# Kernel tuning notes

Hardware: AMD Instinct MI355X
Metric: run time of the kernel (lower is better)

Reference implementation:

```python
import jax, jax.numpy as jnp
import numpy as np

N_HEAD = 16


def setup_inputs() -> dict:
    key = jax.random.key(0)
    ks = jax.random.split(key, 5)
    B, S, D = 4, 2048, 1024
    scale = 1.0 / np.sqrt(D)
    return {
        "x": jax.random.normal(ks[0], (B, S, D), dtype=jnp.float32),
        "Wq": jax.random.normal(ks[1], (D, D), dtype=jnp.float32) * scale,
        "bq": jnp.zeros((D,), dtype=jnp.float32),
        "Wk": jax.random.normal(ks[2], (D, D), dtype=jnp.float32) * scale,
        "bk": jnp.zeros((D,), dtype=jnp.float32),
        "Wv": jax.random.normal(ks[3], (D, D), dtype=jnp.float32) * scale,
        "bv": jnp.zeros((D,), dtype=jnp.float32),
        "Wo": jax.random.normal(ks[4], (D, D), dtype=jnp.float32) * scale,
        "bo": jnp.zeros((D,), dtype=jnp.float32),
    }


def reference(x, Wq, bq, Wk, bk, Wv, bv, Wo, bo):
    B, S, D = x.shape
    H = N_HEAD
    Dh = D // H
    # projections (torch Linear == x @ W^T + b; here W stored as (in, out))
    q = (x @ Wq + bq).reshape(B, S, H, Dh).transpose(0, 2, 1, 3)  # (B,H,S,Dh)
    k = (x @ Wk + bk).reshape(B, S, H, Dh).transpose(0, 2, 1, 3)
    v = (x @ Wv + bv).reshape(B, S, H, Dh).transpose(0, 2, 1, 3)
    scores = jnp.einsum("bhsd,bhtd->bhst", q, k) / jnp.sqrt(jnp.float32(Dh))
    causal = jnp.tril(jnp.ones((S, S), dtype=bool))  # (S,S)
    scores = jnp.where(causal[None, None], scores, -jnp.inf)
    weights = jax.nn.softmax(scores, axis=-1)  # (B,H,S,S)
    attn = jnp.einsum("bhst,bhtd->bhsd", weights, v)
    attn = attn.transpose(0, 2, 1, 3).reshape(B, S, D)
    out = attn @ Wo + bo
    return out
```

## Files before the change

kernel.cpp:

```cpp
#include <hip/hip_runtime.h>
#include <hip/hip_bf16.h>


typedef __bf16 bf16x8 __attribute__((ext_vector_type(8)));
typedef float f32x4 __attribute__((ext_vector_type(4)));
typedef unsigned short u16;

__device__ __forceinline__ u16 f2b(float f) {
    __hip_bfloat16 h = __float2bfloat16(f);
    return __builtin_bit_cast(unsigned short, h);
}

__device__ __forceinline__ f32x4 mfma16(bf16x8 a, bf16x8 b, f32x4 c) {
    return __builtin_amdgcn_mfma_f32_16x16x32_bf16(a, b, c, 0, 0, 0);
}

typedef const __attribute__((address_space(1))) unsigned int* gas1_t;
typedef __attribute__((address_space(3))) unsigned int* las3_t;
__device__ __forceinline__ void gld16(const void* g, void* l) {
    __builtin_amdgcn_global_load_lds((gas1_t)g, (las3_t)l, 16, 0, 0);
}

__global__ __launch_bounds__(256) void convert_x(const float* __restrict__ x,
                                                 u16* __restrict__ xb, int n4) {
    int i = blockIdx.x * 256 + threadIdx.x;
    if (i < n4) {
        float4 v = ((const float4*)x)[i];
        ushort4 u;
        u.x = f2b(v.x); u.y = f2b(v.y); u.z = f2b(v.z); u.w = f2b(v.w);
        ((ushort4*)xb)[i] = u;
    }
}

__global__ __launch_bounds__(256) void transpose_w(const float* __restrict__ Wq,
                                                   const float* __restrict__ Wk,
                                                   const float* __restrict__ Wv,
                                                   const float* __restrict__ Wo,
                                                   u16* __restrict__ wqkvt,
                                                   u16* __restrict__ wot) {
    const int z = blockIdx.z;
    const float* src = (z == 0) ? Wq : (z == 1) ? Wk : (z == 2) ? Wv : Wo;
    u16* dst = (z == 3) ? wot : (wqkvt + (size_t)z * 1024 * 1024);
    __shared__ float tile[32][33];
    const int tx = threadIdx.x, ty = threadIdx.y;
    const int nbase = blockIdx.x * 32, kbase = blockIdx.y * 32;
    for (int j = 0; j < 4; ++j)
        tile[ty + j * 8][tx] = src[(size_t)(kbase + ty + j * 8) * 1024 + nbase + tx];
    __syncthreads();
    for (int j = 0; j < 4; ++j)
        dst[(size_t)(nbase + ty + j * 8) * 1024 + kbase + tx] = f2b(tile[tx][ty + j * 8]);
}

__global__ __launch_bounds__(256) void pack_bqkv(const float* __restrict__ bq,
                                                 const float* __restrict__ bk,
                                                 const float* __restrict__ bv,
                                                 float* __restrict__ bqkv) {
    int i = blockIdx.x * 256 + threadIdx.x;
    bqkv[i] = (i < 1024) ? bq[i] : (i < 2048) ? bk[i - 1024] : bv[i - 2048];
}

template <int MODE>
__global__ __launch_bounds__(256, 2) void gemm_bt(const u16* __restrict__ A,
                                                  const u16* __restrict__ Bt,
                                                  const float* __restrict__ bias,
                                                  void* __restrict__ Cout,
                                                  void* __restrict__ Cout2,
                                                  int M, int N, int K, int ldc) {
    const int tid = threadIdx.x;
    const int l = tid & 63;
    const int w = tid >> 6;
    const int tileM = blockIdx.x * 128;
    const int tileN = blockIdx.y * 128;

    __shared__ u16 As[2][128 * 32];
    __shared__ u16 Bs[2][128 * 32];

    const int srow = l >> 2;
    const int schunk = l & 3;
    const int mrow = l & 15;
    const int g8 = (l >> 4) * 8;
    const int waveM = (w & 1) * 64;
    const int waveN = (w >> 1) * 64;

    const u16* a0 = A + (size_t)(tileM + w * 32 + srow) * K + schunk * 8;
    const u16* a1 = A + (size_t)(tileM + w * 32 + 16 + srow) * K + schunk * 8;
    const u16* b0 = Bt + (size_t)(tileN + w * 32 + srow) * K + schunk * 8;
    const u16* b1 = Bt + (size_t)(tileN + w * 32 + 16 + srow) * K + schunk * 8;

    f32x4 acc[4][4] = {};

    gld16(a0, &As[0][(w * 2) * 512]);
    gld16(a1, &As[0][(w * 2 + 1) * 512]);
    gld16(b0, &Bs[0][(w * 2) * 512]);
    gld16(b1, &Bs[0][(w * 2 + 1) * 512]);
    __syncthreads();

    for (int k0 = 0; k0 < K; k0 += 32) {
        const int cur = (k0 >> 5) & 1;
        if (k0 + 32 < K) {
            const int nb = cur ^ 1;
            gld16(a0 + k0 + 32, &As[nb][(w * 2) * 512]);
            gld16(a1 + k0 + 32, &As[nb][(w * 2 + 1) * 512]);
            gld16(b0 + k0 + 32, &Bs[nb][(w * 2) * 512]);
            gld16(b1 + k0 + 32, &Bs[nb][(w * 2 + 1) * 512]);
        }

        bf16x8 af[4], bf[4];
        for (int im = 0; im < 4; ++im)
            af[im] = *(const bf16x8*)&As[cur][(waveM + im * 16 + mrow) * 32 + g8];
        for (int in = 0; in < 4; ++in)
            bf[in] = *(const bf16x8*)&Bs[cur][(waveN + in * 16 + mrow) * 32 + g8];
        for (int im = 0; im < 4; ++im)
            for (int in = 0; in < 4; ++in)
                acc[im][in] = mfma16(af[im], bf[in], acc[im][in]);
        __syncthreads();
    }

    const int rbase = (l >> 4) * 4;
    for (int im = 0; im < 4; ++im) {
        for (int in = 0; in < 4; ++in) {
            const int gm0 = tileM + waveM + im * 16 + rbase;
            const int gn = tileN + waveN + in * 16 + (l & 15);
            const float bv_ = bias[gn];
            if (MODE == 1) {
                float* out = (float*)Cout;
                for (int r = 0; r < 4; ++r)
                    out[(size_t)(gm0 + r) * ldc + gn] = acc[im][in][r] + bv_;
            } else if (tileN < 2048) {
                const float qs = (tileN < 1024) ? 0.125f * 1.4426950408889634f : 1.0f;
                u16* out = (u16*)Cout;
                for (int r = 0; r < 4; ++r)
                    out[(size_t)(gm0 + r) * 2048 + gn] = f2b((acc[im][in][r] + bv_) * qs);
            } else {
                u16* out = (u16*)Cout2;
                const int b = gm0 >> 11, s0 = gm0 & 2047;
                const int gn2 = gn - 2048;
                const int h = gn2 >> 6, dh = gn2 & 63;
                ushort4 u;
                u.x = f2b(acc[im][in][0] + bv_);
                u.y = f2b(acc[im][in][1] + bv_);
                u.z = f2b(acc[im][in][2] + bv_);
                u.w = f2b(acc[im][in][3] + bv_);
                *(ushort4*)&out[((size_t)((b * 16 + h) * 64 + dh)) * 2048 + s0] = u;
            }
        }
    }
}

__global__ __launch_bounds__(256, 2) void attn_kernel(const u16* __restrict__ qk,
                                                      const u16* __restrict__ vt,
                                                      u16* __restrict__ attn) {
    const int bh = blockIdx.x;
    const int qt = 15 - (int)blockIdx.y;
    const int b = bh >> 4, h = bh & 15;
    const int q0 = qt * 128;
    const int tid = threadIdx.x, l = tid & 63, w = tid >> 6;
    const int q = l & 15;
    const int g = l >> 4;
    const int g8 = g * 8;

    __shared__ u16 Ks[2][64 * 64];
    __shared__ u16 Vs[2][64 * 64];
    __shared__ u16 Ps[128 * 72];

    const int sr8 = l >> 3;
    const int gc = (l & 7) ^ sr8;
    const u16* kgl = qk + (size_t)(b * 2048 + w * 16 + sr8) * 2048 + 1024 + h * 64 + gc * 8;
    const u16* vgl = vt + (size_t)(bh * 64 + w * 16 + sr8) * 2048 + gc * 8;

    for (int i = 0; i < 4; ++i) {
        const int idx = i * 256 + tid;
        const int row = idx >> 3, ch = idx & 7;
        *(uint4*)&Ps[row * 72 + ch * 8] =
            *(const uint4*)&qk[(size_t)(b * 2048 + q0 + row) * 2048 + h * 64 + ch * 8];
    }
    for (int j = 0; j < 2; ++j) {
        gld16(kgl + (size_t)(j * 8) * 2048, &Ks[0][(w * 16 + j * 8) * 64]);
        gld16(vgl + (size_t)(j * 8) * 2048, &Vs[0][(w * 16 + j * 8) * 64]);
    }
    __syncthreads();

    bf16x8 qb[2][2];
    for (int c = 0; c < 2; ++c) {
        qb[c][0] = *(const bf16x8*)&Ps[(w * 32 + c * 16 + q) * 72 + g8];
        qb[c][1] = *(const bf16x8*)&Ps[(w * 32 + c * 16 + q) * 72 + 32 + g8];
    }

    const int cl0 = ((g) ^ (q & 7)) * 8;
    const int cl1 = ((4 + g) ^ (q & 7)) * 8;

    float li[2] = {0.f, 0.f};
    f32x4 o[2][4] = {};
    const int tmax = 2 * qt + 1;
    const int tdiag = (q0 + w * 32 + 31) >> 6;

    for (int t = 0; t <= tmax; ++t) {
        const int tp = (t < tmax) ? t + 1 : tmax;
        const int nb = (t + 1) & 1;
        for (int j = 0; j < 2; ++j) {
            gld16(kgl + (size_t)(tp * 64 + j * 8) * 2048, &Ks[nb][(w * 16 + j * 8) * 64]);
            gld16(vgl + (size_t)(j * 8) * 2048 + tp * 64, &Vs[nb][(w * 16 + j * 8) * 64]);
        }

        if (t <= tdiag) {
            const int cb0 = t & 1;
            const int kv0 = t * 64;
            const u16* ks = &Ks[cb0][0];
            const u16* vs = &Vs[cb0][0];

            f32x4 st[2][4] = {};
            for (int cb = 0; cb < 4; ++cb) {
                bf16x8 ka0 = *(const bf16x8*)&ks[(cb * 16 + q) * 64 + cl0];
                bf16x8 ka1 = *(const bf16x8*)&ks[(cb * 16 + q) * 64 + cl1];
                st[0][cb] = mfma16(ka0, qb[0][0], st[0][cb]);
                st[1][cb] = mfma16(ka0, qb[1][0], st[1][cb]);
                st[0][cb] = mfma16(ka1, qb[0][1], st[0][cb]);
                st[1][cb] = mfma16(ka1, qb[1][1], st[1][cb]);
            }
            for (int c = 0; c < 2; ++c) {
                if (t == tdiag) {
                    const int qg = q0 + w * 32 + c * 16 + q;
                    for (int cb = 0; cb < 4; ++cb)
                        for (int r = 0; r < 4; ++r) {
                            const int key = kv0 + cb * 16 + g * 4 + r;
                            if (key > qg) st[c][cb][r] = -1e30f;
                        }
                }
                float ps = 0.f;
                for (int cb = 0; cb < 4; ++cb)
                    for (int r = 0; r < 4; ++r) {
                        const float p = __builtin_amdgcn_exp2f(st[c][cb][r]);
                        st[c][cb][r] = p;
                        ps += p;
                    }
                li[c] += ps;
                for (int cb = 0; cb < 4; ++cb) {
                    ushort4 u;
                    u.x = f2b(st[c][cb][0]); u.y = f2b(st[c][cb][1]);
                    u.z = f2b(st[c][cb][2]); u.w = f2b(st[c][cb][3]);
                    *(ushort4*)&Ps[(w * 32 + c * 16 + q) * 72 + cb * 16 + g * 4] = u;
                }
            }
            __builtin_amdgcn_s_waitcnt(0xC07F);
            for (int cb = 0; cb < 4; ++cb) {
                bf16x8 va0 = *(const bf16x8*)&vs[(cb * 16 + q) * 64 + cl0];
                bf16x8 va1 = *(const bf16x8*)&vs[(cb * 16 + q) * 64 + cl1];
                bf16x8 pb00 = *(const bf16x8*)&Ps[(w * 32 + q) * 72 + g8];
                bf16x8 pb01 = *(const bf16x8*)&Ps[(w * 32 + q) * 72 + 32 + g8];
                bf16x8 pb10 = *(const bf16x8*)&Ps[(w * 32 + 16 + q) * 72 + g8];
                bf16x8 pb11 = *(const bf16x8*)&Ps[(w * 32 + 16 + q) * 72 + 32 + g8];
                o[0][cb] = mfma16(va0, pb00, o[0][cb]);
                o[1][cb] = mfma16(va0, pb10, o[1][cb]);
                o[0][cb] = mfma16(va1, pb01, o[0][cb]);
                o[1][cb] = mfma16(va1, pb11, o[1][cb]);
            }
        }
        __syncthreads();
    }

    for (int c = 0; c < 2; ++c) {
        float ps = li[c];
        ps += __shfl_xor(ps, 16);
        ps += __shfl_xor(ps, 32);
        const float inv = 1.0f / ps;
        const size_t tok = (size_t)(b * 2048 + q0 + w * 32 + c * 16 + q);
        for (int cb = 0; cb < 4; ++cb) {
            ushort4 u;
            u.x = f2b(o[c][cb][0] * inv); u.y = f2b(o[c][cb][1] * inv);
            u.z = f2b(o[c][cb][2] * inv); u.w = f2b(o[c][cb][3] * inv);
            *(ushort4*)&attn[tok * 1024 + h * 64 + cb * 16 + g * 4] = u;
        }
    }
}

extern "C" void kernel_launch(void* const* d_in, const int* in_sizes, int n_in,
                              void* d_out, int out_size, void* d_ws, size_t ws_size,
                              hipStream_t stream) {
    const float* x  = (const float*)d_in[0];
    const float* Wq = (const float*)d_in[1];
    const float* bq = (const float*)d_in[2];
    const float* Wk = (const float*)d_in[3];
    const float* bk = (const float*)d_in[4];
    const float* Wv = (const float*)d_in[5];
    const float* bv = (const float*)d_in[6];
    const float* Wo = (const float*)d_in[7];
    const float* bo = (const float*)d_in[8];
    float* out = (float*)d_out;

    char* ws = (char*)d_ws;
    size_t off = 0;
    auto alloc = [&](size_t bytes) -> void* {
        void* p = ws + off;
        off += (bytes + 255) & ~(size_t)255;
        return p;
    };
    u16*   xb    = (u16*)alloc(8192ull * 1024 * 2);
    u16*   wqkvt = (u16*)alloc(3072ull * 1024 * 2);
    u16*   wot   = (u16*)alloc(1024ull * 1024 * 2);
    float* bqkv  = (float*)alloc(3072ull * 4);
    u16*   qk    = (u16*)alloc(8192ull * 2048 * 2);
    u16*   vt    = (u16*)alloc(8192ull * 1024 * 2);
    u16*   attn  = (u16*)alloc(8192ull * 1024 * 2);

    convert_x<<<8192, 256, 0, stream>>>(x, xb, 8192 * 1024 / 4);
    transpose_w<<<dim3(32, 32, 4), dim3(32, 8), 0, stream>>>(Wq, Wk, Wv, Wo, wqkvt, wot);
    pack_bqkv<<<12, 256, 0, stream>>>(bq, bk, bv, bqkv);
    gemm_bt<0><<<dim3(64, 24), 256, 0, stream>>>(xb, wqkvt, bqkv, qk, vt, 8192, 3072, 1024, 0);
    attn_kernel<<<dim3(64, 16), 256, 0, stream>>>(qk, vt, attn);
    gemm_bt<1><<<dim3(64, 8), 256, 0, stream>>>(attn, wot, bo, out, nullptr, 8192, 1024, 1024, 1024);
}
```

Baseline: 247.1 us.

## Add 256x256-tile 8-wave QKV projection GEMM with quadrant-pipelined LDS staging

Replaces the 128x128 QKV projection GEMM with a new 512-thread kernel that computes 256x256 output tiles using a K-step of 64. Staging is split into four quadrant phases, interleaving direct global-to-LDS loads with MFMA work under explicit waitcnt, barriers and setprio. The goal is more data reuse per LDS byte and hiding load latency behind compute. In exchange it uses much more LDS (128KB double-buffered), more registers and fewer blocks (384), which may cap occupancy. The hand-tuned waitcnt sequencing also risks race bugs.

```diff
diff --git a/kernel.cpp b/kernel.cpp
--- a/kernel.cpp
+++ b/kernel.cpp
@@ -57,6 +57,161 @@
                                                  float* __restrict__ bqkv) {
     int i = blockIdx.x * 256 + threadIdx.x;
     bqkv[i] = (i < 1024) ? bq[i] : (i < 2048) ? bk[i - 1024] : bv[i - 2048];
+}
+
+__global__ __launch_bounds__(512, 2) void gemm256(const u16* __restrict__ A,
+                                                  const u16* __restrict__ Bt,
+                                                  const float* __restrict__ bias,
+                                                  u16* __restrict__ qkout,
+                                                  u16* __restrict__ vtout,
+                                                  int K) {
+    const int tid = threadIdx.x;
+    const int l = tid & 63;
+    const int w = tid >> 6;
+    const int mw = w >> 1;
+    const int nw = w & 1;
+    const int mrow = l & 15;
+    const int g = l >> 4;
+    const int tileM = blockIdx.x * 256;
+    const int tileN = blockIdx.y * 256;
+
+    __shared__ u16 As[2][256 * 64];
+    __shared__ u16 Bs[2][256 * 64];
+
+    const int swz = mrow & 7;
+    const int co0 = ((0 + g) ^ swz) * 8;
+    const int co1 = ((4 + g) ^ swz) * 8;
+
+    const int gc = (l & 7) ^ (l >> 3);
+    const u16* aStage = A + (size_t)(tileM + (l >> 3)) * K + gc * 8;
+    const u16* bStage = Bt + (size_t)(tileN + (l >> 3)) * K + gc * 8;
+
+    bf16x8 aR[2][2];
+    bf16x8 bR[4][2];
+    f32x4 acc00[2][4] = {}, acc10[2][4] = {}, acc11[2][4] = {}, acc01[2][4] = {};
+
+    auto stageA = [&](int hh, int tt, int nb) {
+        const u16* p = aStage + (size_t)(hh * 128 + w * 16) * K + tt * 64;
+        gld16(p, &As[nb][(hh * 16 + w * 2) * 512]);
+        gld16(p + (size_t)8 * K, &As[nb][(hh * 16 + w * 2 + 1) * 512]);
+    };
+    auto stageB = [&](int hh, int tt, int nb) {
+        const u16* p = bStage + (size_t)(hh * 128 + w * 16) * K + tt * 64;
+        gld16(p, &Bs[nb][(hh * 16 + w * 2) * 512]);
+        gld16(p + (size_t)8 * K, &Bs[nb][(hh * 16 + w * 2 + 1) * 512]);
+    };
+    auto lda = [&](int qa, int buf) {
+#pragma unroll
+        for (int i2 = 0; i2 < 2; ++i2) {
+            const int r = qa * 128 + mw * 32 + i2 * 16 + mrow;
+            aR[i2][0] = *(const bf16x8*)&As[buf][r * 64 + co0];
+            aR[i2][1] = *(const bf16x8*)&As[buf][r * 64 + co1];
+        }
+    };
+    auto ldb = [&](int qb, int buf) {
+#pragma unroll
+        for (int in = 0; in < 4; ++in) {
+            const int r = qb * 128 + nw * 64 + in * 16 + mrow;
+            bR[in][0] = *(const bf16x8*)&Bs[buf][r * 64 + co0];
+            bR[in][1] = *(const bf16x8*)&Bs[buf][r * 64 + co1];
+        }
+    };
+    auto mm = [&](f32x4 (&C)[2][4]) {
+#pragma unroll
+        for (int ks = 0; ks < 2; ++ks)
+#pragma unroll
+            for (int i2 = 0; i2 < 2; ++i2)
+#pragma unroll
+                for (int in = 0; in < 4; ++in)
+                    C[i2][in] = mfma16(aR[i2][ks], bR[in][ks], C[i2][in]);
+    };
+    auto barSB = [&]() {
+        __builtin_amdgcn_sched_barrier(0);
+        __builtin_amdgcn_s_barrier();
+        __builtin_amdgcn_sched_barrier(0);
+    };
+
+    stageA(0, 0, 0); stageB(0, 0, 0); stageA(1, 0, 0); stageB(1, 0, 0);
+    asm volatile("s_waitcnt vmcnt(4)" ::: "memory");
+    barSB();
+
+    const int NT = K >> 6;
+    for (int t = 0; t < NT; ++t) {
+        const int buf = t & 1, nb = buf ^ 1;
+        const int tp = (t + 1 < NT) ? t + 1 : t;
+
+        lda(0, buf); ldb(0, buf);
+        stageA(0, tp, nb);
+        barSB();
+        asm volatile("s_waitcnt lgkmcnt(0)" ::: "memory");
+        __builtin_amdgcn_sched_barrier(0);
+        __builtin_amdgcn_s_setprio(1);
+        mm(acc00);
+        __builtin_amdgcn_s_setprio(0);
+        asm volatile("s_waitcnt vmcnt(4)" ::: "memory");
+        barSB();
+
+        lda(1, buf);
+        stageB(0, tp, nb);
+        barSB();
+        asm volatile("s_waitcnt lgkmcnt(0)" ::: "memory");
+        __builtin_amdgcn_sched_barrier(0);
+        __builtin_amdgcn_s_setprio(1);
+        mm(acc10);
+        __builtin_amdgcn_s_setprio(0);
+        asm volatile("s_waitcnt vmcnt(4)" ::: "memory");
+        barSB();
+
+        ldb(1, buf);
+        stageA(1, tp, nb);
+        barSB();
+        asm volatile("s_waitcnt lgkmcnt(0)" ::: "memory");
+        __builtin_amdgcn_sched_barrier(0);
+        __builtin_amdgcn_s_setprio(1);
+        mm(acc11);
+        __builtin_amdgcn_s_setprio(0);
+        barSB();
+
+        lda(0, buf);
+        stageB(1, tp, nb);
+        barSB();
+        asm volatile("s_waitcnt lgkmcnt(0)" ::: "memory");
+        __builtin_amdgcn_sched_barrier(0);
+        __builtin_amdgcn_s_setprio(1);
+        mm(acc01);
+        __builtin_amdgcn_s_setprio(0);
+        asm volatile("s_waitcnt vmcnt(4)" ::: "memory");
+        barSB();
+    }
+
+    const int rbase = (l >> 4) * 4;
+    auto epi = [&](f32x4 (&C)[2][4], int qa, int qb) {
+#pragma unroll
+        for (int i2 = 0; i2 < 2; ++i2) {
+#pragma unroll
+            for (int in = 0; in < 4; ++in) {
+                const int gm0 = tileM + qa * 128 + mw * 32 + i2 * 16 + rbase;
+                const int gn = tileN + qb * 128 + nw * 64 + in * 16 + (l & 15);
+                const float bv_ = bias[gn];
+                const f32x4 a = C[i2][in];
+                if (tileN < 2048) {
+                    const float qs = (tileN < 1024) ? 0.125f * 1.4426950408889634f : 1.0f;
+#pragma unroll
+                    for (int r = 0; r < 4; ++r)
+                        qkout[(size_t)(gm0 + r) * 2048 + gn] = f2b((a[r] + bv_) * qs);
+                } else {
+                    const int b = gm0 >> 11, s0 = gm0 & 2047;
+                    const int gn2 = gn - 2048;
+                    const int h = gn2 >> 6, dh = gn2 & 63;
+                    ushort4 u;
+                    u.x = f2b(a[0] + bv_); u.y = f2b(a[1] + bv_);
+                    u.z = f2b(a[2] + bv_); u.w = f2b(a[3] + bv_);
+                    *(ushort4*)&vtout[((size_t)((b * 16 + h) * 64 + dh)) * 2048 + s0] = u;
+                }
+            }
+        }
+    };
+    epi(acc00, 0, 0); epi(acc10, 1, 0); epi(acc11, 1, 1); epi(acc01, 0, 1);
 }
 
 template <int MODE>
@@ -305,7 +460,7 @@
     convert_x<<<8192, 256, 0, stream>>>(x, xb, 8192 * 1024 / 4);
     transpose_w<<<dim3(32, 32, 4), dim3(32, 8), 0, stream>>>(Wq, Wk, Wv, Wo, wqkvt, wot);
     pack_bqkv<<<12, 256, 0, stream>>>(bq, bk, bv, bqkv);
-    gemm_bt<0><<<dim3(64, 24), 256, 0, stream>>>(xb, wqkvt, bqkv, qk, vt, 8192, 3072, 1024, 0);
+    gemm256<<<dim3(32, 12), 512, 0, stream>>>(xb, wqkvt, bqkv, qk, vt, 1024);
     attn_kernel<<<dim3(64, 16), 256, 0, stream>>>(qk, vt, attn);
     gemm_bt<1><<<dim3(64, 8), 256, 0, stream>>>(attn, wot, bo, out, nullptr, 8192, 1024, 1024, 1024);
 }
```

After: 268.0 us. +8.4%, slower.

## Replace QKV projection GEMM with 256x256-tile, 512-thread double-buffered kernel

Applied to the files above, without the earlier changes.

Adds a new GEMM kernel for the fused QKV projection that uses 256x256 output tiles with 8 waves, each computing 64x128. Loads go directly to LDS with XOR-swizzled layout, and staging of the next K-slice is interleaved with MFMA issue under raised priority. Larger tiles raise arithmetic intensity and cut global traffic per FLOP. The cost is more LDS (128KB) and more accumulator registers per thread, which can limit occupancy, and the grid shrinks to 384 blocks for 256 CUs, which may cause tail imbalance.

```diff
diff --git a/kernel.cpp b/kernel.cpp
--- a/kernel.cpp
+++ b/kernel.cpp
@@ -57,6 +57,106 @@
                                                  float* __restrict__ bqkv) {
     int i = blockIdx.x * 256 + threadIdx.x;
     bqkv[i] = (i < 1024) ? bq[i] : (i < 2048) ? bk[i - 1024] : bv[i - 2048];
+}
+
+__global__ __launch_bounds__(512, 2) void gemm256(const u16* __restrict__ A,
+                                                  const u16* __restrict__ Bt,
+                                                  const float* __restrict__ bias,
+                                                  u16* __restrict__ qkout,
+                                                  u16* __restrict__ vtout,
+                                                  int K) {
+    const int tid = threadIdx.x;
+    const int l = tid & 63;
+    const int w = tid >> 6;
+    const int mw = w >> 1;
+    const int nw = w & 1;
+    const int mrow = l & 15;
+    const int tileM = blockIdx.x * 256;
+    const int tileN = blockIdx.y * 256;
+
+    __shared__ u16 As[2][2][256 * 32];
+    __shared__ u16 Bs[2][2][256 * 32];
+
+    const int rco = ((l >> 4) ^ (l & 3)) * 8;
+
+    const int srow = l >> 2;
+    const int scg = (l & 3) ^ (srow & 3);
+    const u16* aSt = A + (size_t)(tileM + w * 16 + srow) * K + scg * 8;
+    const u16* bSt = Bt + (size_t)(tileN + w * 16 + srow) * K + scg * 8;
+
+    f32x4 acc[4][8] = {};
+
+    auto stageAB = [&](int ks, int tt, int nb) {
+        const size_t ko = (size_t)(ks * 32 + tt * 64);
+        gld16(aSt + ko, &As[nb][ks][(w * 16) * 32]);
+        gld16(aSt + (size_t)128 * K + ko, &As[nb][ks][(128 + w * 16) * 32]);
+        gld16(bSt + ko, &Bs[nb][ks][(w * 16) * 32]);
+        gld16(bSt + (size_t)128 * K + ko, &Bs[nb][ks][(128 + w * 16) * 32]);
+    };
+
+    auto phase = [&](int ks, int buf, int tp) {
+        asm volatile("s_waitcnt vmcnt(4)" ::: "memory");
+        __builtin_amdgcn_s_barrier();
+        asm volatile("" ::: "memory");
+        bf16x8 aR[4], bR[8];
+#pragma unroll
+        for (int i = 0; i < 4; ++i) {
+            const int r = mw * 64 + i * 16 + mrow;
+            aR[i] = *(const bf16x8*)&As[buf][ks][r * 32 + rco];
+        }
+#pragma unroll
+        for (int j = 0; j < 8; ++j) {
+            const int r = nw * 128 + j * 16 + mrow;
+            bR[j] = *(const bf16x8*)&Bs[buf][ks][r * 32 + rco];
+        }
+        stageAB(ks, tp, buf ^ 1);
+        __builtin_amdgcn_s_setprio(1);
+#pragma unroll
+        for (int i = 0; i < 4; ++i)
+#pragma unroll
+            for (int j = 0; j < 8; ++j)
+                acc[i][j] = mfma16(aR[i], bR[j], acc[i][j]);
+        __builtin_amdgcn_s_setprio(0);
+    };
+
+    stageAB(0, 0, 0);
+    asm volatile("" ::: "memory");
+    stageAB(1, 0, 0);
+
+    const int NT = K >> 6;
+    for (int t = 0; t < NT; ++t) {
+        const int buf = t & 1;
+        const int tp = (t + 1 < NT) ? t + 1 : t;
+        phase(0, buf, tp);
+        phase(1, buf, tp);
+    }
+    asm volatile("s_waitcnt vmcnt(0)" ::: "memory");
+
+    const int rbase = (l >> 4) * 4;
+#pragma unroll
+    for (int i = 0; i < 4; ++i) {
+#pragma unroll
+        for (int j = 0; j < 8; ++j) {
+            const int gm0 = tileM + mw * 64 + i * 16 + rbase;
+            const int gn = tileN + nw * 128 + j * 16 + (l & 15);
+            const float bv_ = bias[gn];
+            const f32x4 a = acc[i][j];
+            if (tileN < 2048) {
+                const float qs = (tileN < 1024) ? 0.125f * 1.4426950408889634f : 1.0f;
+#pragma unroll
+                for (int r = 0; r < 4; ++r)
+                    qkout[(size_t)(gm0 + r) * 2048 + gn] = f2b((a[r] + bv_) * qs);
+            } else {
+                const int b = gm0 >> 11, s0 = gm0 & 2047;
+                const int gn2 = gn - 2048;
+                const int h = gn2 >> 6, dh = gn2 & 63;
+                ushort4 u;
+                u.x = f2b(a[0] + bv_); u.y = f2b(a[1] + bv_);
+                u.z = f2b(a[2] + bv_); u.w = f2b(a[3] + bv_);
+                *(ushort4*)&vtout[((size_t)((b * 16 + h) * 64 + dh)) * 2048 + s0] = u;
+            }
+        }
+    }
 }
 
 template <int MODE>
@@ -305,7 +405,7 @@
     convert_x<<<8192, 256, 0, stream>>>(x, xb, 8192 * 1024 / 4);
     transpose_w<<<dim3(32, 32, 4), dim3(32, 8), 0, stream>>>(Wq, Wk, Wv, Wo, wqkvt, wot);
     pack_bqkv<<<12, 256, 0, stream>>>(bq, bk, bv, bqkv);
-    gemm_bt<0><<<dim3(64, 24), 256, 0, stream>>>(xb, wqkvt, bqkv, qk, vt, 8192, 3072, 1024, 0);
+    gemm256<<<dim3(32, 12), 512, 0, stream>>>(xb, wqkvt, bqkv, qk, vt, 1024);
     attn_kernel<<<dim3(64, 16), 256, 0, stream>>>(qk, vt, attn);
     gemm_bt<1><<<dim3(64, 8), 256, 0, stream>>>(attn, wot, bo, out, nullptr, 8192, 1024, 1024, 1024);
 }
```

After: 258.1 us. 1.04x slower.
